# Performance work log

Measured on AMD Instinct MI355X. Metric: run time of the kernel, lower is better.

Reference implementation:

```python
import jax, jax.numpy as jnp
import numpy as np

N_NODES = 50000
N_EDGES = 800000
D_IN, D_H1, D_H2 = 256, 128, 64


def setup_inputs() -> dict:
    key = jax.random.key(0)
    k1, k2, k3, k4, k5, k6, k7 = jax.random.split(key, 7)
    x = jax.random.normal(k1, (N_NODES, D_IN), dtype=jnp.float32)
    edge_index = jax.random.randint(k2, (2, N_EDGES), 0, N_NODES, dtype=jnp.int64)
    edge_weight = jax.random.uniform(k3, (N_EDGES,), dtype=jnp.float32)
    # GCNConv params: Linear (no bias) weight + separate bias, Glorot-ish scale
    W1 = jax.random.normal(k4, (D_IN, D_H1), dtype=jnp.float32) / np.sqrt(D_IN)
    b1 = jnp.zeros((D_H1,), dtype=jnp.float32)
    W2 = jax.random.normal(k5, (D_H1, D_H2), dtype=jnp.float32) / np.sqrt(D_H1)
    b2 = jnp.zeros((D_H2,), dtype=jnp.float32)
    return {"x": x, "edge_index": edge_index, "edge_weight": edge_weight,
            "W1": W1, "b1": b1, "W2": W2, "b2": b2}


def _gcn_norm(edge_index, edge_weight, n_nodes):
    # PyG gcn_norm: add self-loops (weight 1), symmetric D^-1/2 A D^-1/2
    loops = jnp.arange(n_nodes, dtype=edge_index.dtype)
    src = jnp.concatenate([edge_index[0], loops])
    dst = jnp.concatenate([edge_index[1], loops])
    w = jnp.concatenate([edge_weight, jnp.ones((n_nodes,), edge_weight.dtype)])
    deg = jax.ops.segment_sum(w, dst, num_segments=n_nodes)
    dinv = jnp.where(deg > 0, jax.lax.rsqrt(deg), 0.0)
    norm = dinv[src] * w * dinv[dst]  # [E+N]
    return src, dst, norm


def _gcn_conv(h, src, dst, norm, W, b, n_nodes):
    h = h @ W                                   # [N, d_out] dense GEMM
    msg = h[src] * norm[:, None]                # gather + scale  [E+N, d_out]
    out = jax.ops.segment_sum(msg, dst, num_segments=n_nodes)  # scatter-add
    return out + b


def reference(x, edge_index, edge_weight, W1, b1, W2, b2):
    n = x.shape[0]
    src, dst, norm = _gcn_norm(edge_index, edge_weight, n)
    # dropout p=0 -> identity
    h = jax.nn.relu(_gcn_conv(x, src, dst, norm, W1, b1, n))
    h = jax.nn.relu(_gcn_conv(h, src, dst, norm, W2, b2, n))
    return h
```

## Files before the change

kernel.cpp:

```cpp
#include <hip/hip_runtime.h>


static constexpr int SCAN_CHUNK = 1024;
static constexpr int CPAD = 16;

using short8 = __attribute__((ext_vector_type(8))) short;
using f32x4  = __attribute__((ext_vector_type(4))) float;

__device__ inline unsigned short bf16rne(float f) {
  unsigned u = __float_as_uint(f);
  u += 0x7fffu + ((u >> 16) & 1u);
  return (unsigned short)(u >> 16);
}
__device__ inline float bflo(unsigned u) { return __uint_as_float(u << 16); }
__device__ inline float bfhi(unsigned u) { return __uint_as_float(u & 0xffff0000u); }

__device__ inline void wtp_pack(const float* __restrict__ W,
                                unsigned short* __restrict__ Wtp,
                                int i, int K, int C) {
  int e = i & 7;
  int l = (i >> 3) & 63;
  int rest = i >> 9;
  int NT = C / 16;
  int nt = rest % NT;
  int kc = rest / NT;
  int k = kc * 32 + (l >> 4) * 8 + e;
  int n = nt * 16 + (l & 15);
  Wtp[i] = bf16rne(W[(size_t)k * C + n]);
}

__global__ __launch_bounds__(256) void k_prep(int* __restrict__ cnt, int nz,
                                              const float* __restrict__ W1,
                                              unsigned short* __restrict__ wtp1,
                                              const float* __restrict__ W2,
                                              unsigned short* __restrict__ wtp2) {
  int i = blockIdx.x * 256 + threadIdx.x;
  if (i < nz) cnt[i] = 0;
  if (i < 256 * 128) wtp_pack(W1, wtp1, i, 256, 128);
  if (i < 128 * 64) wtp_pack(W2, wtp2, i, 128, 64);
}

__global__ __launch_bounds__(256, 4) void k_count_gemm1(
    const int* __restrict__ dst, int* __restrict__ cnt, int* __restrict__ epos,
    int E, int CB,
    const float* __restrict__ A, const unsigned short* __restrict__ Wtp,
    unsigned short* __restrict__ H, int n) {
  const int bid = blockIdx.x;
  const int wid = bid >> 1;
  if ((bid & 1) == 0) {
    const int base = wid * 1024 + threadIdx.x;
    int d[4];
#pragma unroll
    for (int j = 0; j < 4; ++j) {
      int e = base + j * 256;
      d[j] = (e < E) ? dst[e] : -1;
    }
#pragma unroll
    for (int j = 0; j < 4; ++j) {
      int e = base + j * 256;
      if (e < E) epos[e] = atomicAdd(&cnt[(size_t)d[j] * CPAD], 1);
    }
    return;
  }
  constexpr int K = 256, C = 128, NT = C / 16, KCH = K / 32;
  const int w = threadIdx.x >> 6;
  const int l = threadIdx.x & 63;
  const int lm = l & 15;
  const int lk = (l >> 4) * 8;
  const int row0 = (wid * 4 + w) * 16;
  if (row0 >= n) return;
  const int m = row0 + lm;
  const bool valid = m < n;
  const size_t arow = (size_t)(valid ? m : 0) * K;

  short8 af[KCH];
  {
    float4 a[2 * KCH];
#pragma unroll
    for (int c = 0; c < KCH; ++c) {
      if (valid) {
        a[2 * c]     = *(const float4*)(A + arow + c * 32 + lk);
        a[2 * c + 1] = *(const float4*)(A + arow + c * 32 + lk + 4);
      } else {
        a[2 * c] = a[2 * c + 1] = make_float4(0.f, 0.f, 0.f, 0.f);
      }
    }
#pragma unroll
    for (int c = 0; c < KCH; ++c) {
      af[c][0] = (short)bf16rne(a[2 * c].x);     af[c][1] = (short)bf16rne(a[2 * c].y);
      af[c][2] = (short)bf16rne(a[2 * c].z);     af[c][3] = (short)bf16rne(a[2 * c].w);
      af[c][4] = (short)bf16rne(a[2 * c + 1].x); af[c][5] = (short)bf16rne(a[2 * c + 1].y);
      af[c][6] = (short)bf16rne(a[2 * c + 1].z); af[c][7] = (short)bf16rne(a[2 * c + 1].w);
    }
  }
  f32x4 acc[NT] = {};
  const short8* B = (const short8*)Wtp;
#pragma unroll
  for (int c = 0; c < KCH; ++c)
#pragma unroll
    for (int nt = 0; nt < NT; ++nt)
      acc[nt] = __builtin_amdgcn_mfma_f32_16x16x32_bf16(af[c], B[(c * NT + nt) * 64 + l],
                                                        acc[nt], 0, 0, 0);
  const int orow = row0 + (l >> 4) * 4;
#pragma unroll
  for (int nt = 0; nt < NT; ++nt)
#pragma unroll
    for (int r = 0; r < 4; ++r) {
      int g = orow + r;
      if (g < n) H[(size_t)g * C + nt * 16 + lm] = bf16rne(acc[nt][r]);
    }
}

__global__ __launch_bounds__(256) void k_scan1(const int* __restrict__ in,
                                               int* __restrict__ out,
                                               int* __restrict__ sums, int n) {
  __shared__ int sd[256];
  const int base = blockIdx.x * SCAN_CHUNK;
  const int tid = threadIdx.x;
  int v[4], tot = 0;
#pragma unroll
  for (int j = 0; j < 4; ++j) {
    int idx = base + tid * 4 + j;
    v[j] = (idx < n) ? in[(size_t)idx * CPAD] : 0;
    tot += v[j];
  }
  sd[tid] = tot;
  __syncthreads();
  for (int d = 1; d < 256; d <<= 1) {
    int t = (tid >= d) ? sd[tid - d] : 0;
    __syncthreads();
    sd[tid] += t;
    __syncthreads();
  }
  if (tid == 255) sums[blockIdx.x] = sd[255];
  int run = sd[tid] - tot;
#pragma unroll
  for (int j = 0; j < 4; ++j) {
    int idx = base + tid * 4 + j;
    if (idx < n) out[idx] = run;
    run += v[j];
  }
}

__global__ __launch_bounds__(64) void k_scan2(int* __restrict__ sums, int n) {
  int tid = threadIdx.x;
  int o = (tid < n) ? sums[tid] : 0;
  int v = o;
  for (int d = 1; d < 64; d <<= 1) {
    int t = __shfl_up(v, d, 64);
    if (tid >= d) v += t;
  }
  if (tid < n) sums[tid] = v - o;
}

__global__ __launch_bounds__(256) void k_bucket2(const int* __restrict__ src,
                                                 const int* __restrict__ dst,
                                                 const float* __restrict__ w,
                                                 const int* __restrict__ row_ptr,
                                                 const int* __restrict__ chunks,
                                                 const int* __restrict__ epos,
                                                 int2* __restrict__ csr, int E) {
  int e = blockIdx.x * 256 + threadIdx.x;
  if (e < E) {
    int d = dst[e];
    int pos = row_ptr[d] + chunks[d >> 10] + epos[e];
    csr[pos] = make_int2(src[e], __float_as_int(w[e]));
  }
}

__global__ __launch_bounds__(256) void k_deg_dinv(const int* __restrict__ row_ptr,
                                                  const int* __restrict__ chunks,
                                                  const int2* __restrict__ csr,
                                                  float* __restrict__ dinv, int n) {
  int i = blockIdx.x * 256 + threadIdx.x;
  if (i >= n) return;
  const int e0 = row_ptr[i] + chunks[i >> 10];
  const int e1 = row_ptr[i + 1] + chunks[(i + 1) >> 10];
  float s = 1.0f;
  int e = e0;
  for (; e + 4 <= e1; e += 4) {
    float w0 = __int_as_float(csr[e].y), w1 = __int_as_float(csr[e + 1].y);
    float w2 = __int_as_float(csr[e + 2].y), w3 = __int_as_float(csr[e + 3].y);
    s += (w0 + w1) + (w2 + w3);
  }
  for (; e < e1; ++e) s += __int_as_float(csr[e].y);
  dinv[i] = rsqrtf(s);
}

template <int K, int C>
__global__ __launch_bounds__(256, 4) void k_gemm_bf(
    const unsigned short* __restrict__ A, const unsigned short* __restrict__ Wtp,
    unsigned short* __restrict__ H, int n) {
  constexpr int NT = C / 16, KCH = K / 32;
  const int w = threadIdx.x >> 6;
  const int l = threadIdx.x & 63;
  const int lm = l & 15;
  const int lk = (l >> 4) * 8;
  const int row0 = (blockIdx.x * 4 + w) * 16;
  if (row0 >= n) return;
  const int m = row0 + lm;
  const bool valid = m < n;
  const size_t arow = (size_t)(valid ? m : 0) * K;
  short8 af[KCH];
#pragma unroll
  for (int c = 0; c < KCH; ++c)
    af[c] = valid ? *(const short8*)(A + arow + c * 32 + lk)
                  : short8{0, 0, 0, 0, 0, 0, 0, 0};
  f32x4 acc[NT] = {};
  const short8* B = (const short8*)Wtp;
#pragma unroll
  for (int c = 0; c < KCH; ++c)
#pragma unroll
    for (int nt = 0; nt < NT; ++nt)
      acc[nt] = __builtin_amdgcn_mfma_f32_16x16x32_bf16(af[c], B[(c * NT + nt) * 64 + l],
                                                        acc[nt], 0, 0, 0);
  const int orow = row0 + (l >> 4) * 4;
#pragma unroll
  for (int nt = 0; nt < NT; ++nt)
#pragma unroll
    for (int r = 0; r < 4; ++r) {
      int g = orow + r;
      if (g < n) H[(size_t)g * C + nt * 16 + lm] = bf16rne(acc[nt][r]);
    }
}

template <int C, bool OUTF32>
__global__ __launch_bounds__(256) void k_aggregate(
    const int* __restrict__ row_ptr, const int* __restrict__ chunks,
    const int2* __restrict__ csr, const unsigned short* __restrict__ h,
    const float* __restrict__ dinv, const float* __restrict__ bias,
    void* __restrict__ outp, int n) {
  constexpr int LPN = C / 8;
  constexpr int NPB = 256 / LPN;
  const int g = threadIdx.x % LPN;
  const int i = blockIdx.x * NPB + threadIdx.x / LPN;
  if (i >= n) return;
  const float di = dinv[i];
  const uint4* h4 = (const uint4*)h;
  uint4 hv = h4[(size_t)i * LPN + g];
  float a0 = di * bflo(hv.x), a1 = di * bfhi(hv.x);
  float a2 = di * bflo(hv.y), a3 = di * bfhi(hv.y);
  float a4 = di * bflo(hv.z), a5 = di * bfhi(hv.z);
  float a6 = di * bflo(hv.w), a7 = di * bfhi(hv.w);
  const int e1 = row_ptr[i + 1] + chunks[(i + 1) >> 10];
  int e = row_ptr[i] + chunks[i >> 10];
  for (; e + 8 <= e1; e += 8) {
    int2 c[8];
    uint4 v[8];
    float ds[8];
#pragma unroll
    for (int j = 0; j < 8; ++j) c[j] = csr[e + j];
#pragma unroll
    for (int j = 0; j < 8; ++j) v[j] = h4[(size_t)c[j].x * LPN + g];
#pragma unroll
    for (int j = 0; j < 8; ++j) ds[j] = dinv[c[j].x];
#pragma unroll
    for (int j = 0; j < 8; ++j) {
      float wj = __int_as_float(c[j].y) * ds[j];
      a0 = fmaf(bflo(v[j].x), wj, a0); a1 = fmaf(bfhi(v[j].x), wj, a1);
      a2 = fmaf(bflo(v[j].y), wj, a2); a3 = fmaf(bfhi(v[j].y), wj, a3);
      a4 = fmaf(bflo(v[j].z), wj, a4); a5 = fmaf(bfhi(v[j].z), wj, a5);
      a6 = fmaf(bflo(v[j].w), wj, a6); a7 = fmaf(bfhi(v[j].w), wj, a7);
    }
  }
  for (; e + 4 <= e1; e += 4) {
    int2 c[4];
    uint4 v[4];
    float ds[4];
#pragma unroll
    for (int j = 0; j < 4; ++j) c[j] = csr[e + j];
#pragma unroll
    for (int j = 0; j < 4; ++j) v[j] = h4[(size_t)c[j].x * LPN + g];
#pragma unroll
    for (int j = 0; j < 4; ++j) ds[j] = dinv[c[j].x];
#pragma unroll
    for (int j = 0; j < 4; ++j) {
      float wj = __int_as_float(c[j].y) * ds[j];
      a0 = fmaf(bflo(v[j].x), wj, a0); a1 = fmaf(bfhi(v[j].x), wj, a1);
      a2 = fmaf(bflo(v[j].y), wj, a2); a3 = fmaf(bfhi(v[j].y), wj, a3);
      a4 = fmaf(bflo(v[j].z), wj, a4); a5 = fmaf(bfhi(v[j].z), wj, a5);
      a6 = fmaf(bflo(v[j].w), wj, a6); a7 = fmaf(bfhi(v[j].w), wj, a7);
    }
  }
  for (; e < e1; ++e) {
    int2 c = csr[e];
    float wj = __int_as_float(c.y) * dinv[c.x];
    uint4 v = h4[(size_t)c.x * LPN + g];
    a0 = fmaf(bflo(v.x), wj, a0); a1 = fmaf(bfhi(v.x), wj, a1);
    a2 = fmaf(bflo(v.y), wj, a2); a3 = fmaf(bfhi(v.y), wj, a3);
    a4 = fmaf(bflo(v.z), wj, a4); a5 = fmaf(bfhi(v.z), wj, a5);
    a6 = fmaf(bflo(v.w), wj, a6); a7 = fmaf(bfhi(v.w), wj, a7);
  }
  const float4* b4 = (const float4*)bias;
  float4 bb0 = b4[g * 2], bb1 = b4[g * 2 + 1];
  a0 = fmaxf(fmaf(a0, di, bb0.x), 0.f); a1 = fmaxf(fmaf(a1, di, bb0.y), 0.f);
  a2 = fmaxf(fmaf(a2, di, bb0.z), 0.f); a3 = fmaxf(fmaf(a3, di, bb0.w), 0.f);
  a4 = fmaxf(fmaf(a4, di, bb1.x), 0.f); a5 = fmaxf(fmaf(a5, di, bb1.y), 0.f);
  a6 = fmaxf(fmaf(a6, di, bb1.z), 0.f); a7 = fmaxf(fmaf(a7, di, bb1.w), 0.f);
  if (OUTF32) {
    float4* o4 = (float4*)outp;
    o4[(size_t)i * (C / 4) + g * 2]     = make_float4(a0, a1, a2, a3);
    o4[(size_t)i * (C / 4) + g * 2 + 1] = make_float4(a4, a5, a6, a7);
  } else {
    uint4 o;
    o.x = (unsigned)bf16rne(a0) | ((unsigned)bf16rne(a1) << 16);
    o.y = (unsigned)bf16rne(a2) | ((unsigned)bf16rne(a3) << 16);
    o.z = (unsigned)bf16rne(a4) | ((unsigned)bf16rne(a5) << 16);
    o.w = (unsigned)bf16rne(a6) | ((unsigned)bf16rne(a7) << 16);
    ((uint4*)outp)[(size_t)i * LPN + g] = o;
  }
}

extern "C" void kernel_launch(void* const* d_in, const int* in_sizes, int n_in,
                              void* d_out, int out_size, void* d_ws, size_t ws_size,
                              hipStream_t stream) {
  (void)n_in; (void)out_size; (void)ws_size;
  const float* x  = (const float*)d_in[0];
  const int*   ei = (const int*)d_in[1];
  const float* ew = (const float*)d_in[2];
  const float* W1 = (const float*)d_in[3];
  const float* b1 = (const float*)d_in[4];
  const float* W2 = (const float*)d_in[5];
  const float* b2 = (const float*)d_in[6];
  float* out = (float*)d_out;

  const int N = in_sizes[0] / 256;
  const int E = in_sizes[2];
  const int* src = ei;
  const int* dst = ei + E;

  float* ws      = (float*)d_ws;
  float* dinv    = ws;
  int*   row_ptr = (int*)(ws + 50176);
  int*   chunks  = row_ptr + 50176;
  int*   cnt     = chunks + 256;
  int*   epos    = cnt + 800256;
  int2*  csr     = (int2*)(epos + 800256);
  unsigned short* h1   = (unsigned short*)((int*)csr + 2 * 800256);
  unsigned short* o1   = h1 + (size_t)50000 * 128;
  unsigned short* wtp1 = o1 + (size_t)50000 * 128;
  unsigned short* wtp2 = wtp1 + 128 * 256;
  unsigned short* h2   = h1;

  const int nz = (N + 1) * CPAD;
  const int nchunks = (N + 1 + SCAN_CHUNK - 1) / SCAN_CHUNK;
  const int CB = (E + 1023) / 1024;
  const int GB = (N + 63) / 64;

  k_prep<<<(nz + 255) / 256, 256, 0, stream>>>(cnt, nz, W1, wtp1, W2, wtp2);
  k_count_gemm1<<<CB + GB, 256, 0, stream>>>(dst, cnt, epos, E, CB, x, wtp1, h1, N);
  k_scan1<<<nchunks, 256, 0, stream>>>(cnt, row_ptr, chunks, N + 1);
  k_scan2<<<1, 64, 0, stream>>>(chunks, nchunks);
  k_bucket2<<<(E + 255) / 256, 256, 0, stream>>>(src, dst, ew, row_ptr, chunks,
                                                 epos, csr, E);
  k_deg_dinv<<<(N + 255) / 256, 256, 0, stream>>>(row_ptr, chunks, csr, dinv, N);

  k_aggregate<128, false><<<(N + 15) / 16, 256, 0, stream>>>(row_ptr, chunks, csr,
                                                             h1, dinv, b1, o1, N);
  k_gemm_bf<128, 64><<<(N + 63) / 64, 256, 0, stream>>>(o1, wtp2, h2, N);
  k_aggregate<64, true><<<(N + 31) / 32, 256, 0, stream>>>(row_ptr, chunks, csr,
                                                           h2, dinv, b2, out, N);
}
```

Measured before the change: 136.7 us.

## Fuse layer-1 aggregation with layer-2 GEMM and unpad degree counters

Merges the first-layer neighbor aggregation with the second-layer MFMA GEMM. Each 16-node block writes its aggregated bf16 rows into a swizzled LDS tile and multiplies them by W2 in place, so the o1 intermediate never makes a round trip through global memory and one launch is removed. The degree counter array is no longer padded to 16 ints per node, which cuts memset and scan traffic but makes atomic contention between neighbouring counters more likely. The count/GEMM interleave changes to two count blocks of 512 edges per GEMM block, and the 4-edge unrolled tail in the second aggregation is dropped.

After: 149.0 us. 1.09x slower.

```diff
diff --git a/kernel.cpp b/kernel.cpp
--- a/kernel.cpp
+++ b/kernel.cpp
@@ -2,7 +2,6 @@
 
 
 static constexpr int SCAN_CHUNK = 1024;
-static constexpr int CPAD = 16;
 
 using short8 = __attribute__((ext_vector_type(8))) short;
 using f32x4  = __attribute__((ext_vector_type(4))) float;
@@ -14,6 +13,9 @@
 }
 __device__ inline float bflo(unsigned u) { return __uint_as_float(u << 16); }
 __device__ inline float bfhi(unsigned u) { return __uint_as_float(u & 0xffff0000u); }
+__device__ inline unsigned pk(float lo, float hi) {
+  return (unsigned)bf16rne(lo) | ((unsigned)bf16rne(hi) << 16);
+}
 
 __device__ inline void wtp_pack(const float* __restrict__ W,
                                 unsigned short* __restrict__ Wtp,
@@ -29,45 +31,40 @@
   Wtp[i] = bf16rne(W[(size_t)k * C + n]);
 }
 
-__global__ __launch_bounds__(256) void k_prep(int* __restrict__ cnt, int nz,
+__global__ __launch_bounds__(256) void k_prep(int* __restrict__ cnt, int n1,
                                               const float* __restrict__ W1,
                                               unsigned short* __restrict__ wtp1,
                                               const float* __restrict__ W2,
                                               unsigned short* __restrict__ wtp2) {
   int i = blockIdx.x * 256 + threadIdx.x;
-  if (i < nz) cnt[i] = 0;
+  if (i < n1) cnt[i] = 0;
   if (i < 256 * 128) wtp_pack(W1, wtp1, i, 256, 128);
   if (i < 128 * 64) wtp_pack(W2, wtp2, i, 128, 64);
 }
 
 __global__ __launch_bounds__(256, 4) void k_count_gemm1(
     const int* __restrict__ dst, int* __restrict__ cnt, int* __restrict__ epos,
-    int E, int CB,
+    int E,
     const float* __restrict__ A, const unsigned short* __restrict__ Wtp,
     unsigned short* __restrict__ H, int n) {
   const int bid = blockIdx.x;
-  const int wid = bid >> 1;
-  if ((bid & 1) == 0) {
-    const int base = wid * 1024 + threadIdx.x;
-    int d[4];
-#pragma unroll
-    for (int j = 0; j < 4; ++j) {
-      int e = base + j * 256;
-      d[j] = (e < E) ? dst[e] : -1;
-    }
-#pragma unroll
-    for (int j = 0; j < 4; ++j) {
-      int e = base + j * 256;
-      if (e < E) epos[e] = atomicAdd(&cnt[(size_t)d[j] * CPAD], 1);
-    }
+  const int r3 = bid % 3;
+  if (r3 != 2) {
+    const int cwid = (bid / 3) * 2 + r3;
+    const int base = cwid * 512 + threadIdx.x;
+    int d0 = (base < E) ? dst[base] : -1;
+    int d1 = (base + 256 < E) ? dst[base + 256] : -1;
+    if (base < E) epos[base] = atomicAdd(&cnt[d0], 1);
+    if (base + 256 < E) epos[base + 256] = atomicAdd(&cnt[d1], 1);
     return;
   }
   constexpr int K = 256, C = 128, NT = C / 16, KCH = K / 32;
+  const int gwid = bid / 3;
   const int w = threadIdx.x >> 6;
   const int l = threadIdx.x & 63;
   const int lm = l & 15;
   const int lk = (l >> 4) * 8;
-  const int row0 = (wid * 4 + w) * 16;
+  const int row0 = (gwid * 4 + w) * 16;
   if (row0 >= n) return;
   const int m = row0 + lm;
   const bool valid = m < n;
@@ -121,7 +118,7 @@
 #pragma unroll
   for (int j = 0; j < 4; ++j) {
     int idx = base + tid * 4 + j;
-    v[j] = (idx < n) ? in[(size_t)idx * CPAD] : 0;
+    v[j] = (idx < n) ? in[idx] : 0;
     tot += v[j];
   }
   sd[tid] = tot;
@@ -187,53 +184,100 @@
   dinv[i] = rsqrtf(s);
 }
 
-template <int K, int C>
-__global__ __launch_bounds__(256, 4) void k_gemm_bf(
-    const unsigned short* __restrict__ A, const unsigned short* __restrict__ Wtp,
-    unsigned short* __restrict__ H, int n) {
-  constexpr int NT = C / 16, KCH = K / 32;
+__global__ __launch_bounds__(256) void k_agg1_gemm2(
+    const int* __restrict__ row_ptr, const int* __restrict__ chunks,
+    const int2* __restrict__ csr, const unsigned short* __restrict__ h,
+    const float* __restrict__ dinv, const float* __restrict__ bias,
+    const unsigned short* __restrict__ wtp2, unsigned short* __restrict__ h2,
+    int n) {
+  constexpr int LPN = 16;
+  __shared__ uint4 o_lds[16][16];
+  const int g = threadIdx.x & 15;
+  const int r = threadIdx.x >> 4;
+  const int i = blockIdx.x * 16 + r;
+  const bool valid = i < n;
+  float a0 = 0, a1 = 0, a2 = 0, a3 = 0, a4 = 0, a5 = 0, a6 = 0, a7 = 0;
+  if (valid) {
+    const float di = dinv[i];
+    const uint4* h4 = (const uint4*)h;
+    uint4 hv = h4[(size_t)i * LPN + g];
+    a0 = di * bflo(hv.x); a1 = di * bfhi(hv.x);
+    a2 = di * bflo(hv.y); a3 = di * bfhi(hv.y);
+    a4 = di * bflo(hv.z); a5 = di * bfhi(hv.z);
+    a6 = di * bflo(hv.w); a7 = di * bfhi(hv.w);
+    const int e1 = row_ptr[i + 1] + chunks[(i + 1) >> 10];
+    int e = row_ptr[i] + chunks[i >> 10];
+    for (; e + 8 <= e1; e += 8) {
+      int2 c[8];
+      uint4 v[8];
+      float ds[8];
+#pragma unroll
+      for (int j = 0; j < 8; ++j) c[j] = csr[e + j];
+#pragma unroll
+      for (int j = 0; j < 8; ++j) v[j] = h4[(size_t)c[j].x * LPN + g];
+#pragma unroll
+      for (int j = 0; j < 8; ++j) ds[j] = dinv[c[j].x];
+#pragma unroll
+      for (int j = 0; j < 8; ++j) {
+        float wj = __int_as_float(c[j].y) * ds[j];
+        a0 = fmaf(bflo(v[j].x), wj, a0); a1 = fmaf(bfhi(v[j].x), wj, a1);
+        a2 = fmaf(bflo(v[j].y), wj, a2); a3 = fmaf(bfhi(v[j].y), wj, a3);
+        a4 = fmaf(bflo(v[j].z), wj, a4); a5 = fmaf(bfhi(v[j].z), wj, a5);
+        a6 = fmaf(bflo(v[j].w), wj, a6); a7 = fmaf(bfhi(v[j].w), wj, a7);
+      }
+    }
+    for (; e < e1; ++e) {
+      int2 c = csr[e];
+      float wj = __int_as_float(c.y) * dinv[c.x];
+      uint4 v = h4[(size_t)c.x * LPN + g];
+      a0 = fmaf(bflo(v.x), wj, a0); a1 = fmaf(bfhi(v.x), wj, a1);
+      a2 = fmaf(bflo(v.y), wj, a2); a3 = fmaf(bfhi(v.y), wj, a3);
+      a4 = fmaf(bflo(v.z), wj, a4); a5 = fmaf(bfhi(v.z), wj, a5);
+      a6 = fmaf(bflo(v.w), wj, a6); a7 = fmaf(bfhi(v.w), wj, a7);
+    }
+    const float4* b4 = (const float4*)bias;
+    float4 bb0 = b4[g * 2], bb1 = b4[g * 2 + 1];
+    a0 = fmaxf(fmaf(a0, di, bb0.x), 0.f); a1 = fmaxf(fmaf(a1, di, bb0.y), 0.f);
+    a2 = fmaxf(fmaf(a2, di, bb0.z), 0.f); a3 = fmaxf(fmaf(a3, di, bb0.w), 0.f);
+    a4 = fmaxf(fmaf(a4, di, bb1.x), 0.f); a5 = fmaxf(fmaf(a5, di, bb1.y), 0.f);
+    a6 = fmaxf(fmaf(a6, di, bb1.z), 0.f); a7 = fmaxf(fmaf(a7, di, bb1.w), 0.f);
+  }
+  uint4 o;
+  o.x = pk(a0, a1); o.y = pk(a2, a3); o.z = pk(a4, a5); o.w = pk(a6, a7);
+  o_lds[r][g ^ r] = o;
+  __syncthreads();
   const int w = threadIdx.x >> 6;
   const int l = threadIdx.x & 63;
   const int lm = l & 15;
-  const int lk = (l >> 4) * 8;
-  const int row0 = (blockIdx.x * 4 + w) * 16;
-  if (row0 >= n) return;
-  const int m = row0 + lm;
-  const bool valid = m < n;
-  const size_t arow = (size_t)(valid ? m : 0) * K;
-  short8 af[KCH];
-#pragma unroll
-  for (int c = 0; c < KCH; ++c)
-    af[c] = valid ? *(const short8*)(A + arow + c * 32 + lk)
-                  : short8{0, 0, 0, 0, 0, 0, 0, 0};
-  f32x4 acc[NT] = {};
-  const short8* B = (const short8*)Wtp;
-#pragma unroll
-  for (int c = 0; c < KCH; ++c)
-#pragma unroll
-    for (int nt = 0; nt < NT; ++nt)
-      acc[nt] = __builtin_amdgcn_mfma_f32_16x16x32_bf16(af[c], B[(c * NT + nt) * 64 + l],
-                                                        acc[nt], 0, 0, 0);
-  const int orow = row0 + (l >> 4) * 4;
-#pragma unroll
-  for (int nt = 0; nt < NT; ++nt)
-#pragma unroll
-    for (int r = 0; r < 4; ++r) {
-      int g = orow + r;
-      if (g < n) H[(size_t)g * C + nt * 16 + lm] = bf16rne(acc[nt][r]);
-    }
-}
-
-template <int C, bool OUTF32>
-__global__ __launch_bounds__(256) void k_aggregate(
+  f32x4 acc = {};
+  const short8* B = (const short8*)wtp2;
+#pragma unroll
+  for (int c = 0; c < 4; ++c) {
+    uint4 au = o_lds[lm][(c * 4 + (l >> 4)) ^ lm];
+    short8 af;
+    af[0] = (short)(au.x & 0xffff); af[1] = (short)(au.x >> 16);
+    af[2] = (short)(au.y & 0xffff); af[3] = (short)(au.y >> 16);
+    af[4] = (short)(au.z & 0xffff); af[5] = (short)(au.z >> 16);
+    af[6] = (short)(au.w & 0xffff); af[7] = (short)(au.w >> 16);
+    acc = __builtin_amdgcn_mfma_f32_16x16x32_bf16(af, B[(c * 4 + w) * 64 + l],
+                                                  acc, 0, 0, 0);
+  }
+  const int m0 = (l >> 4) * 4;
+#pragma unroll
+  for (int rr = 0; rr < 4; ++rr) {
+    int grow = blockIdx.x * 16 + m0 + rr;
+    if (grow < n) h2[(size_t)grow * 64 + w * 16 + lm] = bf16rne(acc[rr]);
+  }
+}
+
+__global__ __launch_bounds__(256) void k_aggregate2(
     const int* __restrict__ row_ptr, const int* __restrict__ chunks,
     const int2* __restrict__ csr, const unsigned short* __restrict__ h,
     const float* __restrict__ dinv, const float* __restrict__ bias,
-    void* __restrict__ outp, int n) {
-  constexpr int LPN = C / 8;
-  constexpr int NPB = 256 / LPN;
-  const int g = threadIdx.x % LPN;
-  const int i = blockIdx.x * NPB + threadIdx.x / LPN;
+    float* __restrict__ outp, int n) {
+  constexpr int LPN = 8;
+  const int g = threadIdx.x & 7;
+  const int i = blockIdx.x * 32 + (threadIdx.x >> 3);
   if (i >= n) return;
   const float di = dinv[i];
   const uint4* h4 = (const uint4*)h;
@@ -263,25 +307,6 @@
       a6 = fmaf(bflo(v[j].w), wj, a6); a7 = fmaf(bfhi(v[j].w), wj, a7);
     }
   }
-  for (; e + 4 <= e1; e += 4) {
-    int2 c[4];
-    uint4 v[4];
-    float ds[4];
-#pragma unroll
-    for (int j = 0; j < 4; ++j) c[j] = csr[e + j];
-#pragma unroll
-    for (int j = 0; j < 4; ++j) v[j] = h4[(size_t)c[j].x * LPN + g];
-#pragma unroll
-    for (int j = 0; j < 4; ++j) ds[j] = dinv[c[j].x];
-#pragma unroll
-    for (int j = 0; j < 4; ++j) {
-      float wj = __int_as_float(c[j].y) * ds[j];
-      a0 = fmaf(bflo(v[j].x), wj, a0); a1 = fmaf(bfhi(v[j].x), wj, a1);
-      a2 = fmaf(bflo(v[j].y), wj, a2); a3 = fmaf(bfhi(v[j].y), wj, a3);
-      a4 = fmaf(bflo(v[j].z), wj, a4); a5 = fmaf(bfhi(v[j].z), wj, a5);
-      a6 = fmaf(bflo(v[j].w), wj, a6); a7 = fmaf(bfhi(v[j].w), wj, a7);
-    }
-  }
   for (; e < e1; ++e) {
     int2 c = csr[e];
     float wj = __int_as_float(c.y) * dinv[c.x];
@@ -293,22 +318,13 @@
   }
   const float4* b4 = (const float4*)bias;
   float4 bb0 = b4[g * 2], bb1 = b4[g * 2 + 1];
-  a0 = fmaxf(fmaf(a0, di, bb0.x), 0.f); a1 = fmaxf(fmaf(a1, di, bb0.y), 0.f);
-  a2 = fmaxf(fmaf(a2, di, bb0.z), 0.f); a3 = fmaxf(fmaf(a3, di, bb0.w), 0.f);
-  a4 = fmaxf(fmaf(a4, di, bb1.x), 0.f); a5 = fmaxf(fmaf(a5, di, bb1.y), 0.f);
-  a6 = fmaxf(fmaf(a6, di, bb1.z), 0.f); a7 = fmaxf(fmaf(a7, di, bb1.w), 0.f);
-  if (OUTF32) {
-    float4* o4 = (float4*)outp;
-    o4[(size_t)i * (C / 4) + g * 2]     = make_float4(a0, a1, a2, a3);
-    o4[(size_t)i * (C / 4) + g * 2 + 1] = make_float4(a4, a5, a6, a7);
-  } else {
-    uint4 o;
-    o.x = (unsigned)bf16rne(a0) | ((unsigned)bf16rne(a1) << 16);
-    o.y = (unsigned)bf16rne(a2) | ((unsigned)bf16rne(a3) << 16);
-    o.z = (unsigned)bf16rne(a4) | ((unsigned)bf16rne(a5) << 16);
-    o.w = (unsigned)bf16rne(a6) | ((unsigned)bf16rne(a7) << 16);
-    ((uint4*)outp)[(size_t)i * LPN + g] = o;
-  }
+  float4* o4 = (float4*)outp;
+  o4[(size_t)i * 16 + g * 2] = make_float4(
+      fmaxf(fmaf(a0, di, bb0.x), 0.f), fmaxf(fmaf(a1, di, bb0.y), 0.f),
+      fmaxf(fmaf(a2, di, bb0.z), 0.f), fmaxf(fmaf(a3, di, bb0.w), 0.f));
+  o4[(size_t)i * 16 + g * 2 + 1] = make_float4(
+      fmaxf(fmaf(a4, di, bb1.x), 0.f), fmaxf(fmaf(a5, di, bb1.y), 0.f),
+      fmaxf(fmaf(a6, di, bb1.z), 0.f), fmaxf(fmaf(a7, di, bb1.w), 0.f));
 }
 
 extern "C" void kernel_launch(void* const* d_in, const int* in_sizes, int n_in,
@@ -334,30 +350,29 @@
   int*   row_ptr = (int*)(ws + 50176);
   int*   chunks  = row_ptr + 50176;
   int*   cnt     = chunks + 256;
-  int*   epos    = cnt + 800256;
+  int*   epos    = cnt + 50176;
   int2*  csr     = (int2*)(epos + 800256);
   unsigned short* h1   = (unsigned short*)((int*)csr + 2 * 800256);
-  unsigned short* o1   = h1 + (size_t)50000 * 128;
-  unsigned short* wtp1 = o1 + (size_t)50000 * 128;
+  unsigned short* h2   = h1 + (size_t)50000 * 128;
+  unsigned short* wtp1 = h2 + (size_t)50000 * 64;
   unsigned short* wtp2 = wtp1 + 128 * 256;
-  unsigned short* h2   = h1;
-
-  const int nz = (N + 1) * CPAD;
+
   const int nchunks = (N + 1 + SCAN_CHUNK - 1) / SCAN_CHUNK;
-  const int CB = (E + 1023) / 1024;
+  const int CB = (E + 511) / 512;
   const int GB = (N + 63) / 64;
-
-  k_prep<<<(nz + 255) / 256, 256, 0, stream>>>(cnt, nz, W1, wtp1, W2, wtp2);
-  k_count_gemm1<<<CB + GB, 256, 0, stream>>>(dst, cnt, epos, E, CB, x, wtp1, h1, N);
+  const int P1B = ((CB + 1) / 2) * 3;
+
+  k_prep<<<(N + 1 + 255) / 256, 256, 0, stream>>>(cnt, N + 1, W1, wtp1, W2, wtp2);
+  k_count_gemm1<<<P1B, 256, 0, stream>>>(dst, cnt, epos, E, x, wtp1, h1, N);
   k_scan1<<<nchunks, 256, 0, stream>>>(cnt, row_ptr, chunks, N + 1);
   k_scan2<<<1, 64, 0, stream>>>(chunks, nchunks);
   k_bucket2<<<(E + 255) / 256, 256, 0, stream>>>(src, dst, ew, row_ptr, chunks,
                                                  epos, csr, E);
   k_deg_dinv<<<(N + 255) / 256, 256, 0, stream>>>(row_ptr, chunks, csr, dinv, N);
 
-  k_aggregate<128, false><<<(N + 15) / 16, 256, 0, stream>>>(row_ptr, chunks, csr,
-                                                             h1, dinv, b1, o1, N);
-  k_gemm_bf<128, 64><<<(N + 63) / 64, 256, 0, stream>>>(o1, wtp2, h2, N);
-  k_aggregate<64, true><<<(N + 31) / 32, 256, 0, stream>>>(row_ptr, chunks, csr,
-                                                           h2, dinv, b2, out, N);
-}
+  k_agg1_gemm2<<<(N + 15) / 16, 256, 0, stream>>>(row_ptr, chunks, csr, h1, dinv,
+                                                  b1, wtp2, h2, N);
+  k_aggregate2<<<(N + 31) / 32, 256, 0, stream>>>(row_ptr, chunks, csr, h2, dinv,
+                                                  b2, out, N);
+  (void)GB;
+}
```

## Replace global atomic degree count with per-chunk LDS histograms and column scan

Applied to the files above, without the earlier changes.

Edge counting by destination no longer uses global atomics on padded counters. Each of 256 edge chunks now builds a packed 16-bit-per-node histogram in shared memory, writes it out, and a column-wise scan over chunks produces per-chunk offsets that the bucket kernel uses to place edges. The first GEMM is split back into its own kernel instead of being interleaved with counting, and h2 gets its own buffer. This trades global atomic contention for a large histogram array (256 x 25k words) that must be written, scanned and read, plus one extra launch.

After: 175.5 us. 1.28x slower.

```diff
diff --git a/kernel.cpp b/kernel.cpp
--- a/kernel.cpp
+++ b/kernel.cpp
@@ -2,7 +2,8 @@
 
 
 static constexpr int SCAN_CHUNK = 1024;
-static constexpr int CPAD = 16;
+static constexpr int NCHK = 256;
+static constexpr int LDSW = 25088;
 
 using short8 = __attribute__((ext_vector_type(8))) short;
 using f32x4  = __attribute__((ext_vector_type(4))) float;
@@ -29,45 +30,103 @@
   Wtp[i] = bf16rne(W[(size_t)k * C + n]);
 }
 
-__global__ __launch_bounds__(256) void k_prep(int* __restrict__ cnt, int nz,
-                                              const float* __restrict__ W1,
+__global__ __launch_bounds__(256) void k_prep(const float* __restrict__ W1,
                                               unsigned short* __restrict__ wtp1,
                                               const float* __restrict__ W2,
                                               unsigned short* __restrict__ wtp2) {
   int i = blockIdx.x * 256 + threadIdx.x;
-  if (i < nz) cnt[i] = 0;
   if (i < 256 * 128) wtp_pack(W1, wtp1, i, 256, 128);
   if (i < 128 * 64) wtp_pack(W2, wtp2, i, 128, 64);
 }
 
-__global__ __launch_bounds__(256, 4) void k_count_gemm1(
-    const int* __restrict__ dst, int* __restrict__ cnt, int* __restrict__ epos,
-    int E, int CB,
+__global__ __launch_bounds__(256) void k_hist(const int* __restrict__ dst,
+                                              unsigned* __restrict__ epos,
+                                              unsigned* __restrict__ hist_g,
+                                              int E, int CEDGE, int nwords) {
+  __shared__ unsigned lh[LDSW];
+  for (int i = threadIdx.x; i < LDSW; i += 256) lh[i] = 0;
+  __syncthreads();
+  const int c = blockIdx.x;
+  const int e0 = c * CEDGE;
+  const int e1 = min(e0 + CEDGE, E);
+  for (int e = e0 + threadIdx.x; e < e1; e += 256) {
+    int d = dst[e];
+    int sh = (d & 1) * 16;
+    unsigned old = atomicAdd(&lh[d >> 1], 1u << sh);
+    epos[e] = ((old >> sh) & 0xffffu) | ((unsigned)c << 16);
+  }
+  __syncthreads();
+  unsigned* hg = hist_g + (size_t)c * nwords;
+  for (int i = threadIdx.x; i < nwords; i += 256) hg[i] = lh[i];
+}
+
+__global__ __launch_bounds__(256) void k_tscan(unsigned* __restrict__ hist_g,
+                                               int* __restrict__ cnt,
+                                               int nwords) {
+  int w = blockIdx.x * 256 + threadIdx.x;
+  if (w >= nwords) return;
+  unsigned run = 0;
+  for (int c = 0; c < NCHK; ++c) {
+    size_t idx = (size_t)c * nwords + w;
+    unsigned v = hist_g[idx];
+    hist_g[idx] = run;
+    run += v;
+  }
+  cnt[2 * w] = run & 0xffffu;
+  cnt[2 * w + 1] = run >> 16;
+}
+
+__global__ __launch_bounds__(256) void k_scan1(const int* __restrict__ in,
+                                               int* __restrict__ out,
+                                               int* __restrict__ sums, int n) {
+  __shared__ int sd[256];
+  const int base = blockIdx.x * SCAN_CHUNK;
+  const int tid = threadIdx.x;
+  int v[4], tot = 0;
+#pragma unroll
+  for (int j = 0; j < 4; ++j) {
+    int idx = base + tid * 4 + j;
+    v[j] = (idx < n) ? in[idx] : 0;
+    tot += v[j];
+  }
+  sd[tid] = tot;
+  __syncthreads();
+  for (int d = 1; d < 256; d <<= 1) {
+    int t = (tid >= d) ? sd[tid - d] : 0;
+    __syncthreads();
+    sd[tid] += t;
+    __syncthreads();
+  }
+  if (tid == 255) sums[blockIdx.x] = sd[255];
+  int run = sd[tid] - tot;
+#pragma unroll
+  for (int j = 0; j < 4; ++j) {
+    int idx = base + tid * 4 + j;
+    if (idx < n) out[idx] = run;
+    run += v[j];
+  }
+}
+
+__global__ __launch_bounds__(64) void k_scan2(int* __restrict__ sums, int n) {
+  int tid = threadIdx.x;
+  int o = (tid < n) ? sums[tid] : 0;
+  int v = o;
+  for (int d = 1; d < 64; d <<= 1) {
+    int t = __shfl_up(v, d, 64);
+    if (tid >= d) v += t;
+  }
+  if (tid < n) sums[tid] = v - o;
+}
+
+__global__ __launch_bounds__(256, 4) void k_gemm_f32(
     const float* __restrict__ A, const unsigned short* __restrict__ Wtp,
     unsigned short* __restrict__ H, int n) {
-  const int bid = blockIdx.x;
-  const int wid = bid >> 1;
-  if ((bid & 1) == 0) {
-    const int base = wid * 1024 + threadIdx.x;
-    int d[4];
-#pragma unroll
-    for (int j = 0; j < 4; ++j) {
-      int e = base + j * 256;
-      d[j] = (e < E) ? dst[e] : -1;
-    }
-#pragma unroll
-    for (int j = 0; j < 4; ++j) {
-      int e = base + j * 256;
-      if (e < E) epos[e] = atomicAdd(&cnt[(size_t)d[j] * CPAD], 1);
-    }
-    return;
-  }
   constexpr int K = 256, C = 128, NT = C / 16, KCH = K / 32;
   const int w = threadIdx.x >> 6;
   const int l = threadIdx.x & 63;
   const int lm = l & 15;
   const int lk = (l >> 4) * 8;
-  const int row0 = (wid * 4 + w) * 16;
+  const int row0 = (blockIdx.x * 4 + w) * 16;
   if (row0 >= n) return;
   const int m = row0 + lm;
   const bool valid = m < n;
@@ -111,59 +170,24 @@
     }
 }
 
-__global__ __launch_bounds__(256) void k_scan1(const int* __restrict__ in,
-                                               int* __restrict__ out,
-                                               int* __restrict__ sums, int n) {
-  __shared__ int sd[256];
-  const int base = blockIdx.x * SCAN_CHUNK;
-  const int tid = threadIdx.x;
-  int v[4], tot = 0;
-#pragma unroll
-  for (int j = 0; j < 4; ++j) {
-    int idx = base + tid * 4 + j;
-    v[j] = (idx < n) ? in[(size_t)idx * CPAD] : 0;
-    tot += v[j];
-  }
-  sd[tid] = tot;
-  __syncthreads();
-  for (int d = 1; d < 256; d <<= 1) {
-    int t = (tid >= d) ? sd[tid - d] : 0;
-    __syncthreads();
-    sd[tid] += t;
-    __syncthreads();
-  }
-  if (tid == 255) sums[blockIdx.x] = sd[255];
-  int run = sd[tid] - tot;
-#pragma unroll
-  for (int j = 0; j < 4; ++j) {
-    int idx = base + tid * 4 + j;
-    if (idx < n) out[idx] = run;
-    run += v[j];
-  }
-}
-
-__global__ __launch_bounds__(64) void k_scan2(int* __restrict__ sums, int n) {
-  int tid = threadIdx.x;
-  int o = (tid < n) ? sums[tid] : 0;
-  int v = o;
-  for (int d = 1; d < 64; d <<= 1) {
-    int t = __shfl_up(v, d, 64);
-    if (tid >= d) v += t;
-  }
-  if (tid < n) sums[tid] = v - o;
-}
-
-__global__ __launch_bounds__(256) void k_bucket2(const int* __restrict__ src,
-                                                 const int* __restrict__ dst,
-                                                 const float* __restrict__ w,
-                                                 const int* __restrict__ row_ptr,
-                                                 const int* __restrict__ chunks,
-                                                 const int* __restrict__ epos,
-                                                 int2* __restrict__ csr, int E) {
+__global__ __launch_bounds__(256) void k_bucket(const int* __restrict__ src,
+                                                const int* __restrict__ dst,
+                                                const float* __restrict__ w,
+                                                const int* __restrict__ row_ptr,
+                                                const int* __restrict__ chunks,
+                                                const unsigned* __restrict__ epos,
+                                                const unsigned* __restrict__ hist_g,
+                                                int2* __restrict__ csr, int E,
+                                                int nwords) {
   int e = blockIdx.x * 256 + threadIdx.x;
   if (e < E) {
     int d = dst[e];
-    int pos = row_ptr[d] + chunks[d >> 10] + epos[e];
+    unsigned ep = epos[e];
+    int c = ep >> 16;
+    int rank = ep & 0xffffu;
+    unsigned pw = hist_g[(size_t)c * nwords + (d >> 1)];
+    int cbase = (pw >> ((d & 1) * 16)) & 0xffffu;
+    int pos = row_ptr[d] + chunks[d >> 10] + cbase + rank;
     csr[pos] = make_int2(src[e], __float_as_int(w[e]));
   }
 }
@@ -329,30 +353,33 @@
   const int* src = ei;
   const int* dst = ei + E;
 
-  float* ws      = (float*)d_ws;
-  float* dinv    = ws;
-  int*   row_ptr = (int*)(ws + 50176);
-  int*   chunks  = row_ptr + 50176;
-  int*   cnt     = chunks + 256;
-  int*   epos    = cnt + 800256;
-  int2*  csr     = (int2*)(epos + 800256);
+  const int nwords = (N + 1) >> 1;
+  const int CEDGE = (E + NCHK - 1) / NCHK;
+
+  float*    ws      = (float*)d_ws;
+  float*    dinv    = ws;
+  int*      row_ptr = (int*)(ws + 50176);
+  int*      chunks  = row_ptr + 50176;
+  int*      cnt     = chunks + 256;
+  unsigned* epos    = (unsigned*)(cnt + 50176);
+  unsigned* hist_g  = epos + 800256;
+  int2*     csr     = (int2*)(hist_g + 6400256);
   unsigned short* h1   = (unsigned short*)((int*)csr + 2 * 800256);
   unsigned short* o1   = h1 + (size_t)50000 * 128;
-  unsigned short* wtp1 = o1 + (size_t)50000 * 128;
+  unsigned short* h2   = o1 + (size_t)50000 * 128;
+  unsigned short* wtp1 = h2 + (size_t)50000 * 64;
   unsigned short* wtp2 = wtp1 + 128 * 256;
-  unsigned short* h2   = h1;
-
-  const int nz = (N + 1) * CPAD;
+
   const int nchunks = (N + 1 + SCAN_CHUNK - 1) / SCAN_CHUNK;
-  const int CB = (E + 1023) / 1024;
-  const int GB = (N + 63) / 64;
-
-  k_prep<<<(nz + 255) / 256, 256, 0, stream>>>(cnt, nz, W1, wtp1, W2, wtp2);
-  k_count_gemm1<<<CB + GB, 256, 0, stream>>>(dst, cnt, epos, E, CB, x, wtp1, h1, N);
+
+  k_prep<<<128, 256, 0, stream>>>(W1, wtp1, W2, wtp2);
+  k_hist<<<NCHK, 256, 0, stream>>>(dst, epos, hist_g, E, CEDGE, nwords);
+  k_tscan<<<(nwords + 255) / 256, 256, 0, stream>>>(hist_g, cnt, nwords);
   k_scan1<<<nchunks, 256, 0, stream>>>(cnt, row_ptr, chunks, N + 1);
   k_scan2<<<1, 64, 0, stream>>>(chunks, nchunks);
-  k_bucket2<<<(E + 255) / 256, 256, 0, stream>>>(src, dst, ew, row_ptr, chunks,
-                                                 epos, csr, E);
+  k_gemm_f32<<<(N + 63) / 64, 256, 0, stream>>>(x, wtp1, h1, N);
+  k_bucket<<<(E + 255) / 256, 256, 0, stream>>>(src, dst, ew, row_ptr, chunks,
+                                                epos, hist_g, csr, E, nwords);
   k_deg_dinv<<<(N + 255) / 256, 256, 0, stream>>>(row_ptr, chunks, csr, dinv, N);
 
   k_aggregate<128, false><<<(N + 15) / 16, 256, 0, stream>>>(row_ptr, chunks, csr,
```

## Co-schedule layer-1 GEMM with CSR bucket scatter instead of edge counting

Applied to the files above, without the earlier changes.

Splits the combined count+GEMM kernel into a standalone atomic counting kernel. The first-layer dense GEMM now runs inside the bucket-scatter kernel, with blocks interleaved 4 scatter to 1 GEMM. The goal is to overlap the compute-bound MFMA GEMM with the memory-bound scatter phase rather than the atomic count phase. The scatter grid size is now tied to the node count, so it only covers every edge while E <= 4*256*ceil(N/64), which holds for these input sizes.

Result: slower. 149.8 us (+9.6%).

```diff
diff --git a/kernel.cpp b/kernel.cpp
--- a/kernel.cpp
+++ b/kernel.cpp
@@ -40,34 +40,91 @@
   if (i < 128 * 64) wtp_pack(W2, wtp2, i, 128, 64);
 }
 
-__global__ __launch_bounds__(256, 4) void k_count_gemm1(
-    const int* __restrict__ dst, int* __restrict__ cnt, int* __restrict__ epos,
-    int E, int CB,
+__global__ __launch_bounds__(256) void k_count(const int* __restrict__ dst,
+                                               int* __restrict__ cnt,
+                                               int* __restrict__ epos, int E) {
+  const int base = blockIdx.x * 1024 + threadIdx.x;
+  int d[4];
+#pragma unroll
+  for (int j = 0; j < 4; ++j) {
+    int e = base + j * 256;
+    d[j] = (e < E) ? dst[e] : -1;
+  }
+#pragma unroll
+  for (int j = 0; j < 4; ++j) {
+    int e = base + j * 256;
+    if (e < E) epos[e] = atomicAdd(&cnt[(size_t)d[j] * CPAD], 1);
+  }
+}
+
+__global__ __launch_bounds__(256) void k_scan1(const int* __restrict__ in,
+                                               int* __restrict__ out,
+                                               int* __restrict__ sums, int n) {
+  __shared__ int sd[256];
+  const int base = blockIdx.x * SCAN_CHUNK;
+  const int tid = threadIdx.x;
+  int v[4], tot = 0;
+#pragma unroll
+  for (int j = 0; j < 4; ++j) {
+    int idx = base + tid * 4 + j;
+    v[j] = (idx < n) ? in[(size_t)idx * CPAD] : 0;
+    tot += v[j];
+  }
+  sd[tid] = tot;
+  __syncthreads();
+  for (int d = 1; d < 256; d <<= 1) {
+    int t = (tid >= d) ? sd[tid - d] : 0;
+    __syncthreads();
+    sd[tid] += t;
+    __syncthreads();
+  }
+  if (tid == 255) sums[blockIdx.x] = sd[255];
+  int run = sd[tid] - tot;
+#pragma unroll
+  for (int j = 0; j < 4; ++j) {
+    int idx = base + tid * 4 + j;
+    if (idx < n) out[idx] = run;
+    run += v[j];
+  }
+}
+
+__global__ __launch_bounds__(64) void k_scan2(int* __restrict__ sums, int n) {
+  int tid = threadIdx.x;
+  int o = (tid < n) ? sums[tid] : 0;
+  int v = o;
+  for (int d = 1; d < 64; d <<= 1) {
+    int t = __shfl_up(v, d, 64);
+    if (tid >= d) v += t;
+  }
+  if (tid < n) sums[tid] = v - o;
+}
+
+__global__ __launch_bounds__(256, 4) void k_bucket_gemm1(
+    const int* __restrict__ src, const int* __restrict__ dst,
+    const float* __restrict__ w, const int* __restrict__ row_ptr,
+    const int* __restrict__ chunks, const int* __restrict__ epos,
+    int2* __restrict__ csr, int E,
     const float* __restrict__ A, const unsigned short* __restrict__ Wtp,
     unsigned short* __restrict__ H, int n) {
   const int bid = blockIdx.x;
-  const int wid = bid >> 1;
-  if ((bid & 1) == 0) {
-    const int base = wid * 1024 + threadIdx.x;
-    int d[4];
-#pragma unroll
-    for (int j = 0; j < 4; ++j) {
-      int e = base + j * 256;
-      d[j] = (e < E) ? dst[e] : -1;
-    }
-#pragma unroll
-    for (int j = 0; j < 4; ++j) {
-      int e = base + j * 256;
-      if (e < E) epos[e] = atomicAdd(&cnt[(size_t)d[j] * CPAD], 1);
+  const int r5 = bid % 5;
+  if (r5 != 4) {
+    const int wid = (bid / 5) * 4 + r5;
+    int e = wid * 256 + threadIdx.x;
+    if (e < E) {
+      int d = dst[e];
+      int pos = row_ptr[d] + chunks[d >> 10] + epos[e];
+      csr[pos] = make_int2(src[e], __float_as_int(w[e]));
     }
     return;
   }
   constexpr int K = 256, C = 128, NT = C / 16, KCH = K / 32;
-  const int w = threadIdx.x >> 6;
+  const int gwid = bid / 5;
+  const int w4 = threadIdx.x >> 6;
   const int l = threadIdx.x & 63;
   const int lm = l & 15;
   const int lk = (l >> 4) * 8;
-  const int row0 = (wid * 4 + w) * 16;
+  const int row0 = (gwid * 4 + w4) * 16;
   if (row0 >= n) return;
   const int m = row0 + lm;
   const bool valid = m < n;
@@ -109,63 +166,6 @@
       int g = orow + r;
       if (g < n) H[(size_t)g * C + nt * 16 + lm] = bf16rne(acc[nt][r]);
     }
-}
-
-__global__ __launch_bounds__(256) void k_scan1(const int* __restrict__ in,
-                                               int* __restrict__ out,
-                                               int* __restrict__ sums, int n) {
-  __shared__ int sd[256];
-  const int base = blockIdx.x * SCAN_CHUNK;
-  const int tid = threadIdx.x;
-  int v[4], tot = 0;
-#pragma unroll
-  for (int j = 0; j < 4; ++j) {
-    int idx = base + tid * 4 + j;
-    v[j] = (idx < n) ? in[(size_t)idx * CPAD] : 0;
-    tot += v[j];
-  }
-  sd[tid] = tot;
-  __syncthreads();
-  for (int d = 1; d < 256; d <<= 1) {
-    int t = (tid >= d) ? sd[tid - d] : 0;
-    __syncthreads();
-    sd[tid] += t;
-    __syncthreads();
-  }
-  if (tid == 255) sums[blockIdx.x] = sd[255];
-  int run = sd[tid] - tot;
-#pragma unroll
-  for (int j = 0; j < 4; ++j) {
-    int idx = base + tid * 4 + j;
-    if (idx < n) out[idx] = run;
-    run += v[j];
-  }
-}
-
-__global__ __launch_bounds__(64) void k_scan2(int* __restrict__ sums, int n) {
-  int tid = threadIdx.x;
-  int o = (tid < n) ? sums[tid] : 0;
-  int v = o;
-  for (int d = 1; d < 64; d <<= 1) {
-    int t = __shfl_up(v, d, 64);
-    if (tid >= d) v += t;
-  }
-  if (tid < n) sums[tid] = v - o;
-}
-
-__global__ __launch_bounds__(256) void k_bucket2(const int* __restrict__ src,
-                                                 const int* __restrict__ dst,
-                                                 const float* __restrict__ w,
-                                                 const int* __restrict__ row_ptr,
-                                                 const int* __restrict__ chunks,
-                                                 const int* __restrict__ epos,
-                                                 int2* __restrict__ csr, int E) {
-  int e = blockIdx.x * 256 + threadIdx.x;
-  if (e < E) {
-    int d = dst[e];
-    int pos = row_ptr[d] + chunks[d >> 10] + epos[e];
-    csr[pos] = make_int2(src[e], __float_as_int(w[e]));
-  }
 }
 
 __global__ __launch_bounds__(256) void k_deg_dinv(const int* __restrict__ row_ptr,
@@ -344,15 +344,14 @@
 
   const int nz = (N + 1) * CPAD;
   const int nchunks = (N + 1 + SCAN_CHUNK - 1) / SCAN_CHUNK;
-  const int CB = (E + 1023) / 1024;
   const int GB = (N + 63) / 64;
 
   k_prep<<<(nz + 255) / 256, 256, 0, stream>>>(cnt, nz, W1, wtp1, W2, wtp2);
-  k_count_gemm1<<<CB + GB, 256, 0, stream>>>(dst, cnt, epos, E, CB, x, wtp1, h1, N);
+  k_count<<<(E + 1023) / 1024, 256, 0, stream>>>(dst, cnt, epos, E);
   k_scan1<<<nchunks, 256, 0, stream>>>(cnt, row_ptr, chunks, N + 1);
   k_scan2<<<1, 64, 0, stream>>>(chunks, nchunks);
-  k_bucket2<<<(E + 255) / 256, 256, 0, stream>>>(src, dst, ew, row_ptr, chunks,
-                                                 epos, csr, E);
+  k_bucket_gemm1<<<GB * 5, 256, 0, stream>>>(src, dst, ew, row_ptr, chunks, epos,
+                                             csr, E, x, wtp1, h1, N);
   k_deg_dinv<<<(N + 255) / 256, 256, 0, stream>>>(row_ptr, chunks, csr, dinv, N);
 
   k_aggregate<128, false><<<(N + 15) / 16, 256, 0, stream>>>(row_ptr, chunks, csr,
```
